# Kernel optimization log

Hardware: AMD Instinct MI355X
Metric: run time of the kernel (lower is better)

The kernel has to match this reference:

```python
import jax, jax.numpy as jnp
import numpy as np

B = 256          # trees in batch
DEPTH = 10       # complete binary tree depth
N_PER = 2**DEPTH - 1   # 1023 nodes per tree, heap (level) order
X = 128
H = 128
C_OUT = 32


def setup_inputs() -> dict:
    key = jax.random.key(0)
    ks = jax.random.split(key, 7)
    def w(k, sh, fan):
        return jax.random.normal(k, sh, jnp.float32) / np.float32(np.sqrt(fan))
    return {
        "feats": jax.random.normal(ks[0], (B * N_PER, X), jnp.float32),
        # roots: heap index 0 of each tree in the flat node array
        "offsets": jnp.arange(B, dtype=jnp.int32) * N_PER,
        "W1": w(ks[1], (H, X), X), "b1": jnp.zeros((H,), jnp.float32),
        "W_iou": w(ks[2], (3 * H, H), H),
        "U_iou": w(ks[3], (3 * H, H), H),
        "b_iou": jnp.zeros((1, 3 * H), jnp.float32),
        "U_f": w(ks[4], (H, H), H), "b_f": jnp.zeros((H,), jnp.float32),
        "W_out": w(ks[5], (C_OUT, H), H), "b_out": jnp.zeros((C_OUT,), jnp.float32),
    }


def _apply_node(iou, b_iou, c_in):
    # apply_node_func: iou = iou + b_iou; c = sigmoid(i)*tanh(u) + c_in; h = sigmoid(o)*tanh(c)
    i, o, u = jnp.split(iou + b_iou, 3, axis=-1)
    c = jax.nn.sigmoid(i) * jnp.tanh(u) + c_in
    h = jax.nn.sigmoid(o) * jnp.tanh(c)
    return h, c


def reference(feats, offsets, W1, b1, W_iou, U_iou, b_iou, U_f, b_f, W_out, b_out):
    # mlp1: Linear + ReLU
    x = jax.nn.relu(feats @ W1.T + b1)                 # (N, H)
    iou_x = (x @ W_iou.T).reshape(B, N_PER, 3 * H)     # W_iou(feats), heap order

    # leaves (deepest level): mailbox empty -> c_in = 0, iou from W_iou(x)
    n_leaf = 2 ** (DEPTH - 1)
    lo = n_leaf - 1
    h_lvl, c_lvl = _apply_node(iou_x[:, lo:lo + n_leaf], b_iou, 0.0)
    c_levels = [c_lvl]

    # propagate level-by-level toward root (fixed fan-in 2 per internal node)
    for lvl in range(DEPTH - 2, -1, -1):
        n = 2 ** lvl
        hc = h_lvl.reshape(B, n, 2, H)                 # gathered child h (mailbox)
        cc = c_lvl.reshape(B, n, 2, H)                 # gathered child c
        h_cat = hc.sum(axis=2)                         # mode='sum' reduce
        f = jax.nn.sigmoid(hc @ U_f.T + b_f)           # per-child forget gates
        c_red = (f * cc).sum(axis=2)
        iou = h_cat @ U_iou.T                          # reduce OVERWRITES node 'iou'
        h_lvl, c_lvl = _apply_node(iou, b_iou, c_red)
        c_levels.append(c_lvl)

    # reassemble heap order: level 0 (root) first
    c_all = jnp.concatenate(c_levels[::-1], axis=1).reshape(B * N_PER, H)
    h_root = c_all[offsets]                            # model returns ndata['c'] at roots
    return h_root @ W_out.T + b_out                    # final fc
```

## Files before the change

kernel.cpp:

```cpp
#include <hip/hip_runtime.h>
#include <hip/hip_bf16.h>


typedef __bf16 bf16x8 __attribute__((ext_vector_type(8)));
typedef float  f32x4  __attribute__((ext_vector_type(4)));

#define MFMA16(a,b,c) __builtin_amdgcn_mfma_f32_16x16x32_bf16((a),(b),(c),0,0,0)

__device__ __forceinline__ float fast_sigmoid(float x){
    return __builtin_amdgcn_rcpf(1.0f + __expf(-x));
}
__device__ __forceinline__ float fast_tanh(float x){
    float ax = fabsf(x);
    float e  = __expf(-2.0f*ax);
    float t  = (1.0f - e) * __builtin_amdgcn_rcpf(1.0f + e);
    return x < 0.0f ? -t : t;
}
__device__ __forceinline__ unsigned pack2bf(float a, float b){
    unsigned short ua = __builtin_bit_cast(unsigned short, (__bf16)a);
    unsigned short ub = __builtin_bit_cast(unsigned short, (__bf16)b);
    return (unsigned)ua | ((unsigned)ub << 16);
}
__device__ __forceinline__ int swzoff(int row, int kByte){
    return row*256 + (kByte ^ ((row & 7) << 4));
}
__device__ __forceinline__ bf16x8 lds_frag(const char* base, int rowBase, int lane, int ks){
    int row = rowBase + (lane & 15);
    int kB  = ks*64 + ((lane >> 4) << 4);
    return *(const bf16x8*)(base + swzoff(row, kB));
}
__device__ __forceinline__ bf16x8 lds_pair_frag(const char* base, int row0, int q, int ks){
    bf16x8 ha = *(const bf16x8*)(base + swzoff(row0,     ks*64 + q*16));
    bf16x8 hb = *(const bf16x8*)(base + swzoff(row0 + 1, ks*64 + q*16));
    bf16x8 t;
    #pragma unroll
    for (int e=0;e<8;++e) t[e] = (__bf16)((float)ha[e] + (float)hb[e]);
    return t;
}
__device__ __forceinline__ bf16x8 gfrag(const float* __restrict__ W, int row, int q, int ks){
    const float* p = W + row*128 + ks*32 + q*8;
    f32x4 lo = *(const f32x4*)p;
    f32x4 hi = *(const f32x4*)(p+4);
    bf16x8 t;
    t[0]=(__bf16)lo[0]; t[1]=(__bf16)lo[1]; t[2]=(__bf16)lo[2]; t[3]=(__bf16)lo[3];
    t[4]=(__bf16)hi[0]; t[5]=(__bf16)hi[1]; t[6]=(__bf16)hi[2]; t[7]=(__bf16)hi[3];
    return t;
}
__device__ __forceinline__ void load_w_lds(char* dst, const float* __restrict__ src,
                                           int rows, int tid){
    int total = rows * 32;
    for (int t = tid; t < total; t += 512){
        int row = t >> 5;
        int kq  = (t & 31) << 2;
        f32x4 v = *(const f32x4*)(src + row*128 + kq);
        unsigned long long val = (unsigned long long)pack2bf(v[0], v[1])
                               | ((unsigned long long)pack2bf(v[2], v[3]) << 32);
        *(unsigned long long*)(dst + swzoff(row, kq*2)) = val;
    }
}

struct UFrags {
    bf16x8 uf[4], ui[4], uo[4], uu[4];
    float bi, bo, bu, bfc;
};

template<int N>
__device__ __forceinline__ void level_step(float (&c)[16][4], const char* childR, char* curR,
                                           const UFrags& W, int lane, int colb2){
    const int q = lane >> 4, r = lane & 15;
    constexpr int NCC = (2*N)/16 > 0 ? (2*N)/16 : 1;
    constexpr int NC  = N/16 > 0 ? N/16 : 1;
    constexpr int REDN = NCC > 2 ? NCC : 2;
    float red[REDN][2];
    #pragma unroll
    for (int t=NCC;t<REDN;++t){ red[t][0]=0.f; red[t][1]=0.f; }
    #pragma unroll
    for (int t=0;t<NCC;++t){
        f32x4 acc = {0.f,0.f,0.f,0.f};
        #pragma unroll
        for (int ks=0;ks<4;++ks)
            acc = MFMA16(lds_frag(childR, 16*t, lane, ks), W.uf[ks], acc);
        red[t][0] = fast_sigmoid(acc[0]+W.bfc)*c[t][0] + fast_sigmoid(acc[1]+W.bfc)*c[t][1];
        red[t][1] = fast_sigmoid(acc[2]+W.bfc)*c[t][2] + fast_sigmoid(acc[3]+W.bfc)*c[t][3];
    }
    #pragma unroll
    for (int tau=0; tau<NC; ++tau){
        #pragma unroll
        for (int mp=0; mp<4; ++mp){
            int s   = 4*q + mp;
            int src = ((s>>1)&3)*16 + r;
            float va = __shfl(red[2*tau  ][mp&1], src, 64);
            float vb = __shfl(red[2*tau+1][mp&1], src, 64);
            c[tau][mp] = (q >= 2) ? vb : va;
        }
    }
    #pragma unroll
    for (int tau=0; tau<NC; ++tau){
        f32x4 ai={0.f,0.f,0.f,0.f}, ao=ai, au=ai;
        #pragma unroll
        for (int ks=0;ks<4;++ks){
            bf16x8 a = lds_pair_frag(childR, 32*tau + 2*r, q, ks);
            ai = MFMA16(a, W.ui[ks], ai);
            ao = MFMA16(a, W.uo[ks], ao);
            au = MFMA16(a, W.uu[ks], au);
        }
        #pragma unroll
        for (int m=0;m<4;++m){
            int row = 16*tau + 4*q + m;
            float cv = fast_sigmoid(ai[m]+W.bi)*fast_tanh(au[m]+W.bu) + c[tau][m];
            float hv = fast_sigmoid(ao[m]+W.bo)*fast_tanh(cv);
            c[tau][m] = cv;
            if (N >= 16 || (4*q + m) < N)
                *(__bf16*)(curR + swzoff(row, colb2)) = (__bf16)hv;
        }
    }
    __syncthreads();
}

__global__ __launch_bounds__(512, 2)
void treelstm_fused(const float* __restrict__ feats,
                    const float* __restrict__ W1,   const float* __restrict__ b1,
                    const float* __restrict__ Wiou, const float* __restrict__ Uiou,
                    const float* __restrict__ biou, const float* __restrict__ Uf,
                    const float* __restrict__ bfv,  const float* __restrict__ Wout,
                    const float* __restrict__ bout, float* __restrict__ out)
{
    extern __shared__ char smem[];
    char* stg1   = smem;
    char* stg2   = smem + 32768;
    char* arenaA = smem + 65536;
    char* w1L    = smem + 131072;

    const int tid  = threadIdx.x;
    const int lane = tid & 63;
    const int wave = tid >> 6;
    const int q    = lane >> 4;
    const int r    = lane & 15;
    const int colw = 16*wave + r;
    const int colb2= 2*colw;
    const int tree = blockIdx.x;

    load_w_lds(w1L, W1, 128, tid);

    UFrags W;
    bf16x8 wi[4], wo[4], wu[4];
    #pragma unroll
    for (int ks=0;ks<4;++ks){
        W.uf[ks] = gfrag(Uf,   colw,     q, ks);
        W.ui[ks] = gfrag(Uiou, colw,     q, ks);
        W.uo[ks] = gfrag(Uiou, 128+colw, q, ks);
        W.uu[ks] = gfrag(Uiou, 256+colw, q, ks);
        wi[ks]   = gfrag(Wiou, colw,     q, ks);
        wo[ks]   = gfrag(Wiou, 128+colw, q, ks);
        wu[ks]   = gfrag(Wiou, 256+colw, q, ks);
    }
    W.bi = biou[colw]; W.bo = biou[128+colw]; W.bu = biou[256+colw]; W.bfc = bfv[colw];
    const float b1c = b1[colw];

    __syncthreads();

    const float* featsT = feats + ((size_t)tree*1023 + 511)*128;
    float c[16][4];

    #pragma unroll
    for (int ci=0; ci<4; ++ci){
        #pragma unroll
        for (int t=0;t<8;++t){
            f32x4 acc = {0.f,0.f,0.f,0.f};
            #pragma unroll
            for (int ks=0;ks<4;++ks){
                const float* p = featsT + (size_t)(ci*128 + t*16 + r)*128 + ks*32 + q*8;
                f32x4 lo = *(const f32x4*)p;
                f32x4 hi = *(const f32x4*)(p+4);
                bf16x8 a;
                a[0]=(__bf16)lo[0]; a[1]=(__bf16)lo[1]; a[2]=(__bf16)lo[2]; a[3]=(__bf16)lo[3];
                a[4]=(__bf16)hi[0]; a[5]=(__bf16)hi[1]; a[6]=(__bf16)hi[2]; a[7]=(__bf16)hi[3];
                acc = MFMA16(a, lds_frag(w1L, 16*wave, lane, ks), acc);
            }
            #pragma unroll
            for (int m=0;m<4;++m){
                float xv = fmaxf(acc[m] + b1c, 0.f);
                *(__bf16*)(stg1 + swzoff(16*t + 4*q + m, colb2)) = (__bf16)xv;
            }
        }
        __syncthreads();
        float c0c[8][4];
        #pragma unroll
        for (int t=0;t<8;++t){
            f32x4 ai={0.f,0.f,0.f,0.f}, ao=ai, au=ai;
            #pragma unroll
            for (int ks=0;ks<4;++ks){
                bf16x8 a = lds_frag(stg1, 16*t, lane, ks);
                ai = MFMA16(a, wi[ks], ai);
                ao = MFMA16(a, wo[ks], ao);
                au = MFMA16(a, wu[ks], au);
            }
            #pragma unroll
            for (int m=0;m<4;++m){
                float cv = fast_sigmoid(ai[m]+W.bi)*fast_tanh(au[m]+W.bu);
                float hv = fast_sigmoid(ao[m]+W.bo)*fast_tanh(cv);
                c0c[t][m] = cv;
                *(__bf16*)(stg2 + swzoff(16*t + 4*q + m, colb2)) = (__bf16)hv;
            }
        }
        __syncthreads();
        float red[8][2];
        #pragma unroll
        for (int t=0;t<8;++t){
            f32x4 acc = {0.f,0.f,0.f,0.f};
            #pragma unroll
            for (int ks=0;ks<4;++ks)
                acc = MFMA16(lds_frag(stg2, 16*t, lane, ks), W.uf[ks], acc);
            red[t][0] = fast_sigmoid(acc[0]+W.bfc)*c0c[t][0] + fast_sigmoid(acc[1]+W.bfc)*c0c[t][1];
            red[t][1] = fast_sigmoid(acc[2]+W.bfc)*c0c[t][2] + fast_sigmoid(acc[3]+W.bfc)*c0c[t][3];
        }
        #pragma unroll
        for (int tau=0;tau<4;++tau){
            #pragma unroll
            for (int mp=0;mp<4;++mp){
                int s   = 4*q + mp;
                int src = ((s>>1)&3)*16 + r;
                float va = __shfl(red[2*tau  ][mp&1], src, 64);
                float vb = __shfl(red[2*tau+1][mp&1], src, 64);
                c[4*ci+tau][mp] = (q >= 2) ? vb : va;
            }
        }
        #pragma unroll
        for (int tau=0;tau<4;++tau){
            f32x4 ai={0.f,0.f,0.f,0.f}, ao=ai, au=ai;
            #pragma unroll
            for (int ks=0;ks<4;++ks){
                bf16x8 a = lds_pair_frag(stg2, 32*tau + 2*r, q, ks);
                ai = MFMA16(a, W.ui[ks], ai);
                ao = MFMA16(a, W.uo[ks], ao);
                au = MFMA16(a, W.uu[ks], au);
            }
            #pragma unroll
            for (int m=0;m<4;++m){
                float cv = fast_sigmoid(ai[m]+W.bi)*fast_tanh(au[m]+W.bu) + c[4*ci+tau][m];
                float hv = fast_sigmoid(ao[m]+W.bo)*fast_tanh(cv);
                c[4*ci+tau][m] = cv;
                *(__bf16*)(arenaA + swzoff(64*ci + 16*tau + 4*q + m, colb2)) = (__bf16)hv;
            }
        }
        __syncthreads();
    }

    level_step<128>(c, arenaA, stg1,   W, lane, colb2);
    level_step< 64>(c, stg1,   arenaA, W, lane, colb2);
    level_step< 32>(c, arenaA, stg1,   W, lane, colb2);
    level_step< 16>(c, stg1,   arenaA, W, lane, colb2);
    level_step<  8>(c, arenaA, stg1,   W, lane, colb2);
    level_step<  4>(c, stg1,   arenaA, W, lane, colb2);
    level_step<  2>(c, arenaA, stg1,   W, lane, colb2);
    level_step<  1>(c, stg1,   arenaA, W, lane, colb2);

    float* cbuf = (float*)stg2;
    if (q == 0) cbuf[colw] = c[0][0];
    __syncthreads();
    if (tid < 32){
        float acc = bout[tid];
        const float* wr = Wout + tid*128;
        #pragma unroll
        for (int k=0;k<128;k+=4){
            f32x4 wv = *(const f32x4*)(wr + k);
            acc += wv[0]*cbuf[k] + wv[1]*cbuf[k+1] + wv[2]*cbuf[k+2] + wv[3]*cbuf[k+3];
        }
        out[tree*32 + tid] = acc;
    }
}

extern "C" void kernel_launch(void* const* d_in, const int* in_sizes, int n_in,
                              void* d_out, int out_size, void* d_ws, size_t ws_size,
                              hipStream_t stream)
{
    (void)in_sizes; (void)n_in; (void)out_size; (void)d_ws; (void)ws_size;
    const float* feats = (const float*)d_in[0];
    const float* W1    = (const float*)d_in[2];
    const float* b1    = (const float*)d_in[3];
    const float* Wiou  = (const float*)d_in[4];
    const float* Uiou  = (const float*)d_in[5];
    const float* biou  = (const float*)d_in[6];
    const float* Uf    = (const float*)d_in[7];
    const float* bf    = (const float*)d_in[8];
    const float* Wout  = (const float*)d_in[9];
    const float* bout  = (const float*)d_in[10];
    float* out = (float*)d_out;

    const int lds = 163840;
    hipFuncSetAttribute((const void*)&treelstm_fused,
                        hipFuncAttributeMaxDynamicSharedMemorySize, lds);
    treelstm_fused<<<dim3(256), dim3(512), lds, stream>>>(
        feats, W1, b1, Wiou, Uiou, biou, Uf, bf, Wout, bout, out);
}
```

Baseline: 365.9 us.

## Process leaves in 64-node chunks through two levels, keep W_iou in LDS

The leaf phase now works on 8 chunks of 64 leaves instead of 4 chunks of 128, and each chunk is pushed through two tree levels (leaf, level 8, level 7) before it is stored. This halves the per-thread cell-state array from 16x4 to 8x4. W_iou fragments now come from LDS while W1 fragments are held in registers, which swaps register pressure for extra LDS reads in the leaf iou GEMM. The aim is to cut VGPR use and spills under the 512-thread, 2-blocks-per-CU launch bound, at the cost of more barriers and more LDS traffic.

```diff
diff --git a/kernel.cpp b/kernel.cpp
--- a/kernel.cpp
+++ b/kernel.cpp
@@ -65,7 +65,7 @@
 };
 
 template<int N>
-__device__ __forceinline__ void level_step(float (&c)[16][4], const char* childR, char* curR,
+__device__ __forceinline__ void level_step(float (&c)[8][4], const char* childR, char* curR,
                                            const UFrags& W, int lane, int colb2){
     const int q = lane >> 4, r = lane & 15;
     constexpr int NCC = (2*N)/16 > 0 ? (2*N)/16 : 1;
@@ -126,10 +126,10 @@
                     const float* __restrict__ bout, float* __restrict__ out)
 {
     extern __shared__ char smem[];
-    char* stg1   = smem;
-    char* stg2   = smem + 32768;
-    char* arenaA = smem + 65536;
-    char* w1L    = smem + 131072;
+    char* wiouL = smem;
+    char* stg1  = smem + 98304;
+    char* stg2  = smem + 114688;
+    char* arena = smem + 131072;
 
     const int tid  = threadIdx.x;
     const int lane = tid & 63;
@@ -140,60 +140,54 @@
     const int colb2= 2*colw;
     const int tree = blockIdx.x;
 
-    load_w_lds(w1L, W1, 128, tid);
+    load_w_lds(wiouL, Wiou, 384, tid);
 
     UFrags W;
-    bf16x8 wi[4], wo[4], wu[4];
+    bf16x8 w1f[4];
     #pragma unroll
     for (int ks=0;ks<4;++ks){
         W.uf[ks] = gfrag(Uf,   colw,     q, ks);
         W.ui[ks] = gfrag(Uiou, colw,     q, ks);
         W.uo[ks] = gfrag(Uiou, 128+colw, q, ks);
         W.uu[ks] = gfrag(Uiou, 256+colw, q, ks);
-        wi[ks]   = gfrag(Wiou, colw,     q, ks);
-        wo[ks]   = gfrag(Wiou, 128+colw, q, ks);
-        wu[ks]   = gfrag(Wiou, 256+colw, q, ks);
+        w1f[ks]  = gfrag(W1,   colw,     q, ks);
     }
     W.bi = biou[colw]; W.bo = biou[128+colw]; W.bu = biou[256+colw]; W.bfc = bfv[colw];
     const float b1c = b1[colw];
 
-    __syncthreads();
-
     const float* featsT = feats + ((size_t)tree*1023 + 511)*128;
-    float c[16][4];
-
-    #pragma unroll
-    for (int ci=0; ci<4; ++ci){
-        #pragma unroll
-        for (int t=0;t<8;++t){
+    float c[8][4];
+
+    #pragma unroll
+    for (int ci=0; ci<8; ++ci){
+        #pragma unroll
+        for (int t=0;t<4;++t){
             f32x4 acc = {0.f,0.f,0.f,0.f};
             #pragma unroll
             for (int ks=0;ks<4;++ks){
-                const float* p = featsT + (size_t)(ci*128 + t*16 + r)*128 + ks*32 + q*8;
+                const float* p = featsT + (size_t)(ci*64 + t*16 + r)*128 + ks*32 + q*8;
                 f32x4 lo = *(const f32x4*)p;
                 f32x4 hi = *(const f32x4*)(p+4);
                 bf16x8 a;
                 a[0]=(__bf16)lo[0]; a[1]=(__bf16)lo[1]; a[2]=(__bf16)lo[2]; a[3]=(__bf16)lo[3];
                 a[4]=(__bf16)hi[0]; a[5]=(__bf16)hi[1]; a[6]=(__bf16)hi[2]; a[7]=(__bf16)hi[3];
-                acc = MFMA16(a, lds_frag(w1L, 16*wave, lane, ks), acc);
-            }
-            #pragma unroll
-            for (int m=0;m<4;++m){
-                float xv = fmaxf(acc[m] + b1c, 0.f);
-                *(__bf16*)(stg1 + swzoff(16*t + 4*q + m, colb2)) = (__bf16)xv;
-            }
+                acc = MFMA16(a, w1f[ks], acc);
+            }
+            #pragma unroll
+            for (int m=0;m<4;++m)
+                *(__bf16*)(stg1 + swzoff(16*t + 4*q + m, colb2)) = (__bf16)fmaxf(acc[m]+b1c, 0.f);
         }
         __syncthreads();
-        float c0c[8][4];
-        #pragma unroll
-        for (int t=0;t<8;++t){
+        float c0c[4][4];
+        #pragma unroll
+        for (int t=0;t<4;++t){
             f32x4 ai={0.f,0.f,0.f,0.f}, ao=ai, au=ai;
             #pragma unroll
             for (int ks=0;ks<4;++ks){
                 bf16x8 a = lds_frag(stg1, 16*t, lane, ks);
-                ai = MFMA16(a, wi[ks], ai);
-                ao = MFMA16(a, wo[ks], ao);
-                au = MFMA16(a, wu[ks], au);
+                ai = MFMA16(a, lds_frag(wiouL,       16*wave, lane, ks), ai);
+                ao = MFMA16(a, lds_frag(wiouL, 128 + 16*wave, lane, ks), ao);
+                au = MFMA16(a, lds_frag(wiouL, 256 + 16*wave, lane, ks), au);
             }
             #pragma unroll
             for (int m=0;m<4;++m){
@@ -204,9 +198,9 @@
             }
         }
         __syncthreads();
-        float red[8][2];
-        #pragma unroll
-        for (int t=0;t<8;++t){
+        float red[4][2];
+        #pragma unroll
+        for (int t=0;t<4;++t){
             f32x4 acc = {0.f,0.f,0.f,0.f};
             #pragma unroll
             for (int ks=0;ks<4;++ks)
@@ -214,19 +208,20 @@
             red[t][0] = fast_sigmoid(acc[0]+W.bfc)*c0c[t][0] + fast_sigmoid(acc[1]+W.bfc)*c0c[t][1];
             red[t][1] = fast_sigmoid(acc[2]+W.bfc)*c0c[t][2] + fast_sigmoid(acc[3]+W.bfc)*c0c[t][3];
         }
-        #pragma unroll
-        for (int tau=0;tau<4;++tau){
+        float c8loc[2][4];
+        #pragma unroll
+        for (int tau=0;tau<2;++tau){
             #pragma unroll
             for (int mp=0;mp<4;++mp){
                 int s   = 4*q + mp;
                 int src = ((s>>1)&3)*16 + r;
                 float va = __shfl(red[2*tau  ][mp&1], src, 64);
                 float vb = __shfl(red[2*tau+1][mp&1], src, 64);
-                c[4*ci+tau][mp] = (q >= 2) ? vb : va;
-            }
-        }
-        #pragma unroll
-        for (int tau=0;tau<4;++tau){
+                c8loc[tau][mp] = (q >= 2) ? vb : va;
+            }
+        }
+        #pragma unroll
+        for (int tau=0;tau<2;++tau){
             f32x4 ai={0.f,0.f,0.f,0.f}, ao=ai, au=ai;
             #pragma unroll
             for (int ks=0;ks<4;++ks){
@@ -237,23 +232,60 @@
             }
             #pragma unroll
             for (int m=0;m<4;++m){
-                float cv = fast_sigmoid(ai[m]+W.bi)*fast_tanh(au[m]+W.bu) + c[4*ci+tau][m];
+                float cv = fast_sigmoid(ai[m]+W.bi)*fast_tanh(au[m]+W.bu) + c8loc[tau][m];
                 float hv = fast_sigmoid(ao[m]+W.bo)*fast_tanh(cv);
-                c[4*ci+tau][m] = cv;
-                *(__bf16*)(arenaA + swzoff(64*ci + 16*tau + 4*q + m, colb2)) = (__bf16)hv;
+                c8loc[tau][m] = cv;
+                *(__bf16*)(stg1 + swzoff(16*tau + 4*q + m, colb2)) = (__bf16)hv;
             }
         }
         __syncthreads();
-    }
-
-    level_step<128>(c, arenaA, stg1,   W, lane, colb2);
-    level_step< 64>(c, stg1,   arenaA, W, lane, colb2);
-    level_step< 32>(c, arenaA, stg1,   W, lane, colb2);
-    level_step< 16>(c, stg1,   arenaA, W, lane, colb2);
-    level_step<  8>(c, arenaA, stg1,   W, lane, colb2);
-    level_step<  4>(c, stg1,   arenaA, W, lane, colb2);
-    level_step<  2>(c, arenaA, stg1,   W, lane, colb2);
-    level_step<  1>(c, stg1,   arenaA, W, lane, colb2);
+        float red7[2][2];
+        #pragma unroll
+        for (int t=0;t<2;++t){
+            f32x4 acc = {0.f,0.f,0.f,0.f};
+            #pragma unroll
+            for (int ks=0;ks<4;++ks)
+                acc = MFMA16(lds_frag(stg1, 16*t, lane, ks), W.uf[ks], acc);
+            red7[t][0] = fast_sigmoid(acc[0]+W.bfc)*c8loc[t][0] + fast_sigmoid(acc[1]+W.bfc)*c8loc[t][1];
+            red7[t][1] = fast_sigmoid(acc[2]+W.bfc)*c8loc[t][2] + fast_sigmoid(acc[3]+W.bfc)*c8loc[t][3];
+        }
+        float c7loc[4];
+        #pragma unroll
+        for (int mp=0;mp<4;++mp){
+            int s   = 4*q + mp;
+            int src = ((s>>1)&3)*16 + r;
+            float va = __shfl(red7[0][mp&1], src, 64);
+            float vb = __shfl(red7[1][mp&1], src, 64);
+            c7loc[mp] = (q >= 2) ? vb : va;
+        }
+        {
+            f32x4 ai={0.f,0.f,0.f,0.f}, ao=ai, au=ai;
+            #pragma unroll
+            for (int ks=0;ks<4;++ks){
+                bf16x8 a = lds_pair_frag(stg1, 2*r, q, ks);
+                ai = MFMA16(a, W.ui[ks], ai);
+                ao = MFMA16(a, W.uo[ks], ao);
+                au = MFMA16(a, W.uu[ks], au);
+            }
+            #pragma unroll
+            for (int m=0;m<4;++m){
+                float cv = fast_sigmoid(ai[m]+W.bi)*fast_tanh(au[m]+W.bu) + c7loc[m];
+                float hv = fast_sigmoid(ao[m]+W.bo)*fast_tanh(cv);
+                c[ci][m] = cv;
+                *(__bf16*)(arena + swzoff(16*ci + 4*q + m, colb2)) = (__bf16)hv;
+            }
+        }
+        __syncthreads();
+    }
+
+    char* bufA = wiouL;
+    level_step<64>(c, arena, bufA,  W, lane, colb2);
+    level_step<32>(c, bufA,  arena, W, lane, colb2);
+    level_step<16>(c, arena, bufA,  W, lane, colb2);
+    level_step< 8>(c, bufA,  arena, W, lane, colb2);
+    level_step< 4>(c, arena, bufA,  W, lane, colb2);
+    level_step< 2>(c, bufA,  arena, W, lane, colb2);
+    level_step< 1>(c, arena, bufA,  W, lane, colb2);
 
     float* cbuf = (float*)stg2;
     if (q == 0) cbuf[colw] = c[0][0];
```

New measurement: 370.2 us. No clear change (+1.2%).
